# Optimization experiments

Hardware: AMD Instinct MI355X
Metric: run time of the kernel (lower is better)

Reference implementation:

```python
import jax, jax.numpy as jnp
import numpy as np

N_HEADS = 16


def setup_inputs() -> dict:
    key = jax.random.key(0)
    ks = jax.random.split(key, 6)
    B, S, E = 2, 2048, 1024
    scale = 1.0 / np.sqrt(E)
    return {
        "X": jax.random.normal(ks[0], (B, S, E), dtype=jnp.float32),
        "Wq": jax.random.normal(ks[1], (E, E), dtype=jnp.float32) * scale,
        "Wk": jax.random.normal(ks[2], (E, E), dtype=jnp.float32) * scale,
        "Wv": jax.random.normal(ks[3], (E, E), dtype=jnp.float32) * scale,
        "Wp": jax.random.normal(ks[4], (E, E), dtype=jnp.float32) * scale,
        "bp": jnp.zeros((E,), dtype=jnp.float32),
    }


def reference(X, Wq, Wk, Wv, Wp, bp):
    B, S, E = X.shape
    H = N_HEADS
    dk = E // H
    # qkv projections (Linear with weight [out,in] -> x @ W.T), split heads
    q = (X @ Wq.T).reshape(B, S, H, dk).transpose(0, 2, 1, 3)  # [B,H,S,dk]
    k = (X @ Wk.T).reshape(B, S, H, dk).transpose(0, 2, 1, 3)
    v = (X @ Wv.T).reshape(B, S, H, dk).transpose(0, 2, 1, 3)
    scores = jnp.einsum('bhqd,bhkd->bhqk', q, k) / jnp.sqrt(jnp.asarray(dk, X.dtype))
    causal = jnp.tril(jnp.ones((S, S), dtype=bool))  # [S,S]
    scores = jnp.where(causal[None, None], scores, jnp.asarray(-jnp.inf, X.dtype))
    attn = jax.nn.softmax(scores, axis=-1)  # [B,H,S,S]
    y = jnp.einsum('bhqk,bhkd->bhqd', attn, v)  # [B,H,S,dk]
    y = y.transpose(0, 2, 1, 3).reshape(B, S, E)
    return y @ Wp.T + bp
```

## Files before the change

kernel.cpp:

```cpp
#include <hip/hip_runtime.h>

typedef unsigned short u16;
typedef __bf16 bf16x8 __attribute__((ext_vector_type(8)));
typedef float f32x4 __attribute__((ext_vector_type(4)));
typedef unsigned short u16x8 __attribute__((ext_vector_type(8)));
typedef unsigned short u16x4 __attribute__((ext_vector_type(4)));

union B8 { u16x8 u; bf16x8 b; };

#define MFMA_BF16(a, b, c) __builtin_amdgcn_mfma_f32_16x16x32_bf16((a), (b), (c), 0, 0, 0)

__device__ __forceinline__ u16 f2bf(float f) {
  unsigned x = __float_as_uint(f);
  unsigned r = x + 0x7fffu + ((x >> 16) & 1u);
  return (u16)(r >> 16);
}

__device__ __forceinline__ unsigned cvt_pk_bf16(float lo, float hi) {
  unsigned r;
  asm("v_cvt_pk_bf16_f32 %0, %1, %2" : "=v"(r) : "v"(lo), "v"(hi));
  return r;
}

__device__ __forceinline__ void gl2lds16(const void* g, void* l) {
  __builtin_amdgcn_global_load_lds(
      (const __attribute__((address_space(1))) void*)g,
      (__attribute__((address_space(3))) void*)l, 16, 0, 0);
}

__global__ __launch_bounds__(256) void cast5_kernel(
    const float* __restrict__ X, const float* __restrict__ Wq,
    const float* __restrict__ Wk, const float* __restrict__ Wv,
    const float* __restrict__ Wp, u16* __restrict__ Xb, u16* __restrict__ Wqb,
    u16* __restrict__ Wkb, u16* __restrict__ Wvb, u16* __restrict__ Wpb) {
  size_t i = ((size_t)blockIdx.x * 256 + threadIdx.x) * 4;
  const float* src;
  u16* dst;
  size_t off;
  if (i < 4194304) {
    src = X; dst = Xb; off = i;
  } else if (i < 5242880) {
    src = Wq; dst = Wqb; off = i - 4194304;
  } else if (i < 6291456) {
    src = Wk; dst = Wkb; off = i - 5242880;
  } else if (i < 7340032) {
    src = Wv; dst = Wvb; off = i - 6291456;
  } else {
    src = Wp; dst = Wpb; off = i - 7340032;
  }
  float4 v = *(const float4*)(src + off);
  u16x4 o;
  o[0] = f2bf(v.x); o[1] = f2bf(v.y); o[2] = f2bf(v.z); o[3] = f2bf(v.w);
  *(u16x4*)(dst + off) = o;
}

template <int N0>
__device__ __forceinline__ void mfma16(f32x4 (&acc)[8][4], B8 (&af)[8], B8& b0,
                                       B8& b1) {
  __builtin_amdgcn_s_setprio(1);
#pragma unroll
  for (int m = 0; m < 8; ++m) {
    acc[m][N0] = MFMA_BF16(af[m].b, b0.b, acc[m][N0]);
    acc[m][N0 + 1] = MFMA_BF16(af[m].b, b1.b, acc[m][N0 + 1]);
  }
  __builtin_amdgcn_s_setprio(0);
}

__global__ __launch_bounds__(512, 2) void gemm_qkv256(
    const u16* __restrict__ Xb, const u16* __restrict__ Wb,
    u16* __restrict__ Qb, u16* __restrict__ Kb, u16* __restrict__ Vt) {
  __shared__ __align__(16) u16 Al[2][2][256 * 32];
  __shared__ __align__(16) u16 Bl[2][2][256 * 32];

  int tid = threadIdx.x, lane = tid & 63, w = tid >> 6;
  int wr = w >> 2, wc = w & 3;
  int l16 = lane & 15, lg = lane >> 4;

  int bid = blockIdx.x;
  int swz = (bid & 7) * 24 + (bid >> 3);
  int bm = swz / 12, bn = swz % 12;

  const u16* Ag = Xb + (size_t)bm * 256 * 1024;
  const u16* Bg = Wb + (size_t)bn * 256 * 1024;

  int srow = w * 16 + (lane >> 2);
  int scol = lane & 3;

  auto stA = [&](int buf, int kh, int kt) {
#pragma unroll
    for (int p2 = 0; p2 < 2; ++p2) {
      int r = p2 * 128 + srow;
      int sl = scol ^ ((r >> 1) & 3);
      gl2lds16(Ag + (size_t)r * 1024 + kt * 64 + kh * 32 + sl * 8,
               (char*)&Al[buf][kh][0] + (size_t)(p2 * 128 + w * 16) * 64);
    }
  };
  auto stB = [&](int buf, int kh, int kt) {
#pragma unroll
    for (int p2 = 0; p2 < 2; ++p2) {
      int r = p2 * 128 + srow;
      int sl = scol ^ ((r >> 1) & 3);
      gl2lds16(Bg + (size_t)r * 1024 + kt * 64 + kh * 32 + sl * 8,
               (char*)&Bl[buf][kh][0] + (size_t)(p2 * 128 + w * 16) * 64);
    }
  };
  auto ldA = [&](int buf, int kk, B8 (&af)[8]) {
#pragma unroll
    for (int m = 0; m < 8; ++m) {
      int r = wr * 128 + m * 16 + l16;
      af[m].u = *(const u16x8*)((const char*)&Al[buf][kk][0] + r * 64 +
                                ((lg ^ ((r >> 1) & 3)) << 4));
    }
  };
  auto ldB = [&](int buf, int kk, int nf, B8& bf) {
    int r = wc * 64 + nf * 16 + l16;
    bf.u = *(const u16x8*)((const char*)&Bl[buf][kk][0] + r * 64 +
                           ((lg ^ ((r >> 1) & 3)) << 4));
  };

  f32x4 acc[8][4] = {};

  stA(0, 0, 0); stB(0, 0, 0);
  stA(0, 1, 0); stB(0, 1, 0);
  stA(1, 0, 1); stB(1, 0, 1);
  asm volatile("s_waitcnt vmcnt(8)" ::: "memory");
  __builtin_amdgcn_s_barrier();

  B8 af[8], b0, b1;
  for (int I = 0; I < 8; ++I) {
    int p = 2 * I;
    bool last = (I == 7);
    stA(1, 1, p + 1);
    ldA(0, 0, af); ldB(0, 0, 0, b0); ldB(0, 0, 1, b1);
    mfma16<0>(acc, af, b0, b1);
    stB(1, 1, p + 1);
    ldB(0, 0, 2, b0); ldB(0, 0, 3, b1);
    mfma16<2>(acc, af, b0, b1);
    if (last) asm volatile("s_waitcnt vmcnt(0)" ::: "memory");
    else      asm volatile("s_waitcnt vmcnt(8)" ::: "memory");
    __builtin_amdgcn_s_barrier();
    if (!last) stA(0, 0, p + 2);
    ldA(0, 1, af); ldB(0, 1, 0, b0); ldB(0, 1, 1, b1);
    mfma16<0>(acc, af, b0, b1);
    if (!last) stB(0, 0, p + 2);
    ldB(0, 1, 2, b0); ldB(0, 1, 3, b1);
    mfma16<2>(acc, af, b0, b1);
    if (last) asm volatile("s_waitcnt vmcnt(0)" ::: "memory");
    else      asm volatile("s_waitcnt vmcnt(8)" ::: "memory");
    __builtin_amdgcn_s_barrier();
    if (!last) stA(0, 1, p + 2);
    ldA(1, 0, af); ldB(1, 0, 0, b0); ldB(1, 0, 1, b1);
    mfma16<0>(acc, af, b0, b1);
    if (!last) stB(0, 1, p + 2);
    ldB(1, 0, 2, b0); ldB(1, 0, 3, b1);
    mfma16<2>(acc, af, b0, b1);
    if (last) asm volatile("s_waitcnt vmcnt(0)" ::: "memory");
    else      asm volatile("s_waitcnt vmcnt(8)" ::: "memory");
    __builtin_amdgcn_s_barrier();
    if (!last) stA(1, 0, p + 3);
    ldA(1, 1, af); ldB(1, 1, 0, b0); ldB(1, 1, 1, b1);
    mfma16<0>(acc, af, b0, b1);
    if (!last) stB(1, 0, p + 3);
    ldB(1, 1, 2, b0); ldB(1, 1, 3, b1);
    mfma16<2>(acc, af, b0, b1);
    if (!last) {
      asm volatile("s_waitcnt vmcnt(8)" ::: "memory");
      __builtin_amdgcn_s_barrier();
    }
  }

  const float QSCALE = 0.18033688011112042f;
#pragma unroll
  for (int m = 0; m < 8; ++m)
#pragma unroll
    for (int nf = 0; nf < 4; ++nf) {
      int colg = bn * 256 + wc * 64 + nf * 16 + l16;
      int rowg = bm * 256 + wr * 128 + m * 16 + lg * 4;
      if (bn < 4) {
#pragma unroll
        for (int j = 0; j < 4; ++j)
          Qb[(size_t)(rowg + j) * 1024 + colg] = f2bf(acc[m][nf][j] * QSCALE);
      } else if (bn < 8) {
#pragma unroll
        for (int j = 0; j < 4; ++j)
          Kb[(size_t)(rowg + j) * 1024 + (colg - 1024)] = f2bf(acc[m][nf][j]);
      } else {
        int cv = colg - 2048;
        int hh = cv >> 6, d = cv & 63;
        int bb = rowg >> 11, s0 = rowg & 2047;
        u16x4 pk;
#pragma unroll
        for (int j = 0; j < 4; ++j) pk[j] = f2bf(acc[m][nf][j]);
        *(u16x4*)(Vt + ((size_t)(bb * 16 + hh) * 64 + d) * 2048 + s0) = pk;
      }
    }
}

__global__ __launch_bounds__(256) void gemm_proj_kernel(
    const u16* __restrict__ Y1, const u16* __restrict__ Wpb,
    float* __restrict__ out, const float* __restrict__ bias) {
  __shared__ __align__(16) u16 Asm[2][128 * 64];
  __shared__ __align__(16) u16 Bsm[2][128 * 64];

  const int Kd = 1024, N = 1024;
  int bid = blockIdx.x;
  int swz = (bid & 7) * 32 + (bid >> 3);
  int bm = swz >> 3, bn = swz & 7;
  int tid = threadIdx.x;
  int lane = tid & 63, w = tid >> 6;
  int wr = w >> 1, wc = w & 1;
  int l16 = lane & 15, lg = lane >> 4;

  const u16* Abase = Y1 + (size_t)bm * 128 * Kd;
  const u16* Bbase = Wpb + (size_t)bn * 128 * Kd;

  int r0 = tid >> 3;

  auto stage = [&](int buf, int kt) {
#pragma unroll
    for (int i = 0; i < 4; ++i) {
      int r = i * 32 + r0;
      int sl = (tid & 7) ^ (r & 7);
      gl2lds16(Abase + (size_t)r * Kd + kt * 64 + sl * 8,
               &Asm[buf][i * 2048 + w * 512]);
      gl2lds16(Bbase + (size_t)r * Kd + kt * 64 + sl * 8,
               &Bsm[buf][i * 2048 + w * 512]);
    }
  };

  f32x4 acc[4][4] = {};
  stage(0, 0);
  int buf = 0;

  for (int kt = 0; kt < 16; ++kt) {
    asm volatile("s_waitcnt vmcnt(0)" ::: "memory");
    __syncthreads();
    if (kt + 1 < 16) stage(buf ^ 1, kt + 1);

    B8 af[4][2], bfr[4][2];
#pragma unroll
    for (int mi = 0; mi < 4; ++mi)
#pragma unroll
      for (int kk = 0; kk < 2; ++kk) {
        int r = wr * 64 + mi * 16 + l16;
        int s = kk * 4 + lg;
        af[mi][kk].u = *(const u16x8*)((const char*)&Asm[buf][0] + r * 128 +
                                       ((s ^ (r & 7)) << 4));
      }
#pragma unroll
    for (int ni = 0; ni < 4; ++ni)
#pragma unroll
      for (int kk = 0; kk < 2; ++kk) {
        int r = wc * 64 + ni * 16 + l16;
        int s = kk * 4 + lg;
        bfr[ni][kk].u = *(const u16x8*)((const char*)&Bsm[buf][0] + r * 128 +
                                        ((s ^ (r & 7)) << 4));
      }
    __builtin_amdgcn_s_setprio(1);
#pragma unroll
    for (int mi = 0; mi < 4; ++mi)
#pragma unroll
      for (int ni = 0; ni < 4; ++ni) {
        acc[mi][ni] = MFMA_BF16(af[mi][0].b, bfr[ni][0].b, acc[mi][ni]);
        acc[mi][ni] = MFMA_BF16(af[mi][1].b, bfr[ni][1].b, acc[mi][ni]);
      }
    __builtin_amdgcn_s_setprio(0);
    buf ^= 1;
  }

#pragma unroll
  for (int mi = 0; mi < 4; ++mi)
#pragma unroll
    for (int ni = 0; ni < 4; ++ni) {
      int col = bn * 128 + wc * 64 + ni * 16 + l16;
#pragma unroll
      for (int j = 0; j < 4; ++j) {
        int row = bm * 128 + wr * 64 + mi * 16 + lg * 4 + j;
        out[(size_t)row * N + col] = acc[mi][ni][j] + bias[col];
      }
    }
}

__global__ __launch_bounds__(256, 4) void attn_kernel(const u16* __restrict__ Q,
                                                      const u16* __restrict__ K,
                                                      const u16* __restrict__ Vt,
                                                      u16* __restrict__ Y) {
  __shared__ __align__(16) u16 Kl[2][64 * 64];
  __shared__ __align__(16) u16 Vl[2][64 * 64];
  __shared__ __align__(16) u16 Pl[4][16 * 64];

  const int E = 1024, S = 2048;
  int tid = threadIdx.x;
  int lane = tid & 63, w = tid >> 6;
  int l16 = lane & 15, lg = lane >> 4;
  int h7 = l16 & 7;

  int bid = blockIdx.x;
  int bh = (bid & 7) * 4 + ((bid >> 3) & 3);
  int u = bid >> 5;
  int g = u & 7, kq = u >> 3;
  int qt = (kq == 0) ? 31 - g : (kq == 1) ? 16 + g : (kq == 2) ? 15 - g : g;
  int b = bh >> 4, h = bh & 15;

  const u16* Qb = Q + (size_t)b * S * E + (size_t)h * 64;
  const u16* Kb = K + (size_t)b * S * E + (size_t)h * 64;
  const u16* Vb = Vt + (size_t)bh * 64 * 2048;

  int r0 = tid >> 3;
  int s0 = (tid & 7) ^ (r0 & 7);
  size_t koff = (size_t)r0 * 1024 + s0 * 8;
  size_t voff = (size_t)r0 * 2048 + s0 * 8;
  const u16* kpA = Kb;
  const u16* kpB = Kb + 32 * 1024;
  const u16* vpA = Vb;
  const u16* vpB = Vb + 32 * 2048;

  const char* kbase0 = (const char*)&Kl[0][0] + l16 * 128 + ((lg ^ h7) << 4);
  const char* kbase1 = (const char*)&Kl[0][0] + l16 * 128 + (((4 + lg) ^ h7) << 4);
  const char* vbase0 = (const char*)&Vl[0][0] + l16 * 128 + ((lg ^ h7) << 4);
  const char* vbase1 = (const char*)&Vl[0][0] + l16 * 128 + (((4 + lg) ^ h7) << 4);
  char* pw0 = (char*)&Pl[w][0] + l16 * 128 + (((0 * 2 + (lg >> 1)) ^ h7) << 4) + (lg & 1) * 8;
  char* pw1 = (char*)&Pl[w][0] + l16 * 128 + (((1 * 2 + (lg >> 1)) ^ h7) << 4) + (lg & 1) * 8;
  char* pw2 = (char*)&Pl[w][0] + l16 * 128 + (((2 * 2 + (lg >> 1)) ^ h7) << 4) + (lg & 1) * 8;
  char* pw3 = (char*)&Pl[w][0] + l16 * 128 + (((3 * 2 + (lg >> 1)) ^ h7) << 4) + (lg & 1) * 8;
  const char* pr0 = (const char*)&Pl[w][0] + l16 * 128 + ((lg ^ h7) << 4);
  const char* pr1 = (const char*)&Pl[w][0] + l16 * 128 + (((4 + lg) ^ h7) << 4);

  B8 qa[2];
#pragma unroll
  for (int kk = 0; kk < 2; ++kk)
    qa[kk].u = *(const u16x8*)(Qb + (size_t)(qt * 64 + w * 16 + l16) * E + kk * 32 + lg * 8);

  f32x4 o[4] = {};
  float lrun = 0.f;
  int qrow = w * 16 + l16;

  gl2lds16(kpA + koff, &Kl[0][w * 512]);
  gl2lds16(vpA + voff, &Vl[0][w * 512]);
  gl2lds16(kpB + koff, &Kl[0][2048 + w * 512]);
  gl2lds16(vpB + voff, &Vl[0][2048 + w * 512]);
  kpA += 65536; kpB += 65536; vpA += 64; vpB += 64;

#define ATTN_ITER(BF, DOMASK, DOSTAGE)                                         \
  do {                                                                         \
    asm volatile("s_waitcnt vmcnt(0)" ::: "memory");                           \
    __syncthreads();                                                           \
    if (DOSTAGE) {                                                             \
      gl2lds16(kpA + koff, &Kl[(BF) ^ 1][w * 512]);                            \
      gl2lds16(vpA + voff, &Vl[(BF) ^ 1][w * 512]);                            \
      gl2lds16(kpB + koff, &Kl[(BF) ^ 1][2048 + w * 512]);                     \
      gl2lds16(vpB + voff, &Vl[(BF) ^ 1][2048 + w * 512]);                     \
      kpA += 65536; kpB += 65536; vpA += 64; vpB += 64;                        \
    }                                                                          \
    f32x4 sa[4] = {};                                                          \
    __builtin_amdgcn_s_setprio(1);                                             \
    _Pragma("unroll") for (int nb = 0; nb < 4; ++nb) {                         \
      B8 kf0, kf1;                                                             \
      kf0.u = *(const u16x8*)(kbase0 + (BF)*8192 + nb * 2048);                 \
      kf1.u = *(const u16x8*)(kbase1 + (BF)*8192 + nb * 2048);                 \
      sa[nb] = MFMA_BF16(kf0.b, qa[0].b, sa[nb]);                              \
      sa[nb] = MFMA_BF16(kf1.b, qa[1].b, sa[nb]);                              \
    }                                                                          \
    __builtin_amdgcn_s_setprio(0);                                             \
    float p[16];                                                               \
    _Pragma("unroll") for (int nb = 0; nb < 4; ++nb)                           \
        _Pragma("unroll") for (int j = 0; j < 4; ++j) {                        \
      float pe = __builtin_amdgcn_exp2f(sa[nb][j]);                            \
      if (DOMASK) {                                                            \
        int kv = nb * 16 + lg * 4 + j;                                         \
        if (kv > qrow) pe = 0.f;                                               \
      }                                                                        \
      p[nb * 4 + j] = pe;                                                      \
    }                                                                          \
    {                                                                          \
      union { u16x4 v; unsigned uu[2]; } pk;                                   \
      pk.uu[0] = cvt_pk_bf16(p[0], p[1]);                                      \
      pk.uu[1] = cvt_pk_bf16(p[2], p[3]);                                      \
      *(u16x4*)pw0 = pk.v;                                                     \
      pk.uu[0] = cvt_pk_bf16(p[4], p[5]);                                      \
      pk.uu[1] = cvt_pk_bf16(p[6], p[7]);                                      \
      *(u16x4*)pw1 = pk.v;                                                     \
      pk.uu[0] = cvt_pk_bf16(p[8], p[9]);                                      \
      pk.uu[1] = cvt_pk_bf16(p[10], p[11]);                                    \
      *(u16x4*)pw2 = pk.v;                                                     \
      pk.uu[0] = cvt_pk_bf16(p[12], p[13]);                                    \
      pk.uu[1] = cvt_pk_bf16(p[14], p[15]);                                    \
      *(u16x4*)pw3 = pk.v;                                                     \
    }                                                                          \
    lrun += ((p[0] + p[1]) + (p[2] + p[3])) + ((p[4] + p[5]) + (p[6] + p[7])) +\
            ((p[8] + p[9]) + (p[10] + p[11])) +                                \
            ((p[12] + p[13]) + (p[14] + p[15]));                               \
    B8 pa0, pa1;                                                               \
    pa0.u = *(const u16x8*)pr0;                                                \
    pa1.u = *(const u16x8*)pr1;                                                \
    asm volatile("s_waitcnt lgkmcnt(0)" ::: "memory");                         \
    __builtin_amdgcn_sched_barrier(0);                                         \
    __builtin_amdgcn_s_setprio(1);                                             \
    _Pragma("unroll") for (int nb = 0; nb < 4; ++nb) {                         \
      B8 vf0, vf1;                                                             \
      vf0.u = *(const u16x8*)(vbase0 + (BF)*8192 + nb * 2048);                 \
      vf1.u = *(const u16x8*)(vbase1 + (BF)*8192 + nb * 2048);                 \
      o[nb] = MFMA_BF16(pa0.b, vf0.b, o[nb]);                                  \
      o[nb] = MFMA_BF16(pa1.b, vf1.b, o[nb]);                                  \
    }                                                                          \
    __builtin_amdgcn_s_setprio(0);                                             \
  } while (0)

  int U = qt;
  int i = 0;
  for (; i + 2 <= U; i += 2) {
    ATTN_ITER(0, false, true);
    ATTN_ITER(1, false, true);
  }
  if (U & 1) {
    ATTN_ITER(0, false, true);
    ATTN_ITER(1, true, false);
  } else {
    ATTN_ITER(0, true, false);
  }
#undef ATTN_ITER

  lrun += __shfl_xor(lrun, 16);
  lrun += __shfl_xor(lrun, 32);
  float inv[4];
#pragma unroll
  for (int j = 0; j < 4; ++j) {
    float lj = __shfl(lrun, (lane & 48) | (lg * 4 + j));
    inv[j] = 1.0f / lj;
  }
#pragma unroll
  for (int nb = 0; nb < 4; ++nb)
#pragma unroll
    for (int j = 0; j < 4; ++j) {
      int row = qt * 64 + w * 16 + lg * 4 + j;
      int col = h * 64 + nb * 16 + l16;
      Y[((size_t)b * S + row) * E + col] = f2bf(o[nb][j] * inv[j]);
    }
}

extern "C" void kernel_launch(void* const* d_in, const int* in_sizes, int n_in,
                              void* d_out, int out_size, void* d_ws,
                              size_t ws_size, hipStream_t stream) {
  const float* X = (const float*)d_in[0];
  const float* Wq = (const float*)d_in[1];
  const float* Wk = (const float*)d_in[2];
  const float* Wv = (const float*)d_in[3];
  const float* Wp = (const float*)d_in[4];
  const float* bp = (const float*)d_in[5];
  float* out = (float*)d_out;

  char* ws = (char*)d_ws;
  const size_t MB = 1ull << 20;
  u16* Xb = (u16*)(ws + 0 * MB);
  u16* Wqb = (u16*)(ws + 8 * MB);
  u16* Wkb = (u16*)(ws + 10 * MB);
  u16* Wvb = (u16*)(ws + 12 * MB);
  u16* Wpb = (u16*)(ws + 14 * MB);
  u16* Qb = (u16*)(ws + 16 * MB);
  u16* Kb = (u16*)(ws + 24 * MB);
  u16* VtB = (u16*)(ws + 32 * MB);
  u16* Y1 = (u16*)(ws + 40 * MB);

  cast5_kernel<<<8192, 256, 0, stream>>>(X, Wq, Wk, Wv, Wp, Xb, Wqb, Wkb, Wvb, Wpb);
  gemm_qkv256<<<192, 512, 0, stream>>>(Xb, Wqb, Qb, Kb, VtB);
  attn_kernel<<<1024, 256, 0, stream>>>(Qb, Kb, VtB, Y1);
  gemm_proj_kernel<<<256, 256, 0, stream>>>(Y1, Wpb, out, bp);
}
```

Before: 105.4 us.

## Feed P directly from registers into PV MFMA using 16x16x16 bf16

Removes the per-wave LDS round trip for the probability tile P (write, wait, read back). The bf16-packed exponentials are used directly as A operands of 16x16x16 bf16 MFMAs, with V fragments read in a matching 4-element layout. This drops LDS traffic and the lgkmcnt wait, but doubles the number of PV MFMA instructions (16 smaller ones instead of 8) and uses narrower 8-byte LDS reads for V.

```diff
diff --git a/kernel.cpp b/kernel.cpp
--- a/kernel.cpp
+++ b/kernel.cpp
@@ -9,6 +9,10 @@
 union B8 { u16x8 u; bf16x8 b; };
 
 #define MFMA_BF16(a, b, c) __builtin_amdgcn_mfma_f32_16x16x32_bf16((a), (b), (c), 0, 0, 0)
+
+__device__ __forceinline__ void mfma16x16x16(f32x4& c, u16x4 a, u16x4 b) {
+  asm("v_mfma_f32_16x16x16_bf16 %0, %1, %2, %0" : "+v"(c) : "v"(a), "v"(b));
+}
 
 __device__ __forceinline__ u16 f2bf(float f) {
   unsigned x = __float_as_uint(f);
@@ -287,7 +291,6 @@
                                                       u16* __restrict__ Y) {
   __shared__ __align__(16) u16 Kl[2][64 * 64];
   __shared__ __align__(16) u16 Vl[2][64 * 64];
-  __shared__ __align__(16) u16 Pl[4][16 * 64];
 
   const int E = 1024, S = 2048;
   int tid = threadIdx.x;
@@ -317,14 +320,11 @@
 
   const char* kbase0 = (const char*)&Kl[0][0] + l16 * 128 + ((lg ^ h7) << 4);
   const char* kbase1 = (const char*)&Kl[0][0] + l16 * 128 + (((4 + lg) ^ h7) << 4);
-  const char* vbase0 = (const char*)&Vl[0][0] + l16 * 128 + ((lg ^ h7) << 4);
-  const char* vbase1 = (const char*)&Vl[0][0] + l16 * 128 + (((4 + lg) ^ h7) << 4);
-  char* pw0 = (char*)&Pl[w][0] + l16 * 128 + (((0 * 2 + (lg >> 1)) ^ h7) << 4) + (lg & 1) * 8;
-  char* pw1 = (char*)&Pl[w][0] + l16 * 128 + (((1 * 2 + (lg >> 1)) ^ h7) << 4) + (lg & 1) * 8;
-  char* pw2 = (char*)&Pl[w][0] + l16 * 128 + (((2 * 2 + (lg >> 1)) ^ h7) << 4) + (lg & 1) * 8;
-  char* pw3 = (char*)&Pl[w][0] + l16 * 128 + (((3 * 2 + (lg >> 1)) ^ h7) << 4) + (lg & 1) * 8;
-  const char* pr0 = (const char*)&Pl[w][0] + l16 * 128 + ((lg ^ h7) << 4);
-  const char* pr1 = (const char*)&Pl[w][0] + l16 * 128 + (((4 + lg) ^ h7) << 4);
+  const char* vb64[4];
+#pragma unroll
+  for (int kvs = 0; kvs < 4; ++kvs)
+    vb64[kvs] = (const char*)&Vl[0][0] + l16 * 128 +
+                (((kvs * 2 + (lg >> 1)) ^ h7) << 4) + (lg & 1) * 8;
 
   B8 qa[2];
 #pragma unroll
@@ -362,46 +362,33 @@
       sa[nb] = MFMA_BF16(kf1.b, qa[1].b, sa[nb]);                              \
     }                                                                          \
     __builtin_amdgcn_s_setprio(0);                                             \
-    float p[16];                                                               \
-    _Pragma("unroll") for (int nb = 0; nb < 4; ++nb)                           \
-        _Pragma("unroll") for (int j = 0; j < 4; ++j) {                        \
-      float pe = __builtin_amdgcn_exp2f(sa[nb][j]);                            \
+    u16x4 pa[4];                                                               \
+    float rs = 0.f;                                                            \
+    _Pragma("unroll") for (int nb = 0; nb < 4; ++nb) {                         \
+      float pe0 = __builtin_amdgcn_exp2f(sa[nb][0]);                           \
+      float pe1 = __builtin_amdgcn_exp2f(sa[nb][1]);                           \
+      float pe2 = __builtin_amdgcn_exp2f(sa[nb][2]);                           \
+      float pe3 = __builtin_amdgcn_exp2f(sa[nb][3]);                           \
       if (DOMASK) {                                                            \
-        int kv = nb * 16 + lg * 4 + j;                                         \
-        if (kv > qrow) pe = 0.f;                                               \
+        int kv0 = nb * 16 + lg * 4;                                            \
+        if (kv0 + 0 > qrow) pe0 = 0.f;                                         \
+        if (kv0 + 1 > qrow) pe1 = 0.f;                                         \
+        if (kv0 + 2 > qrow) pe2 = 0.f;                                         \
+        if (kv0 + 3 > qrow) pe3 = 0.f;                                         \
       }                                                                        \
-      p[nb * 4 + j] = pe;                                                      \
+      union { u16x4 v; unsigned uu[2]; } pk;                                   \
+      pk.uu[0] = cvt_pk_bf16(pe0, pe1);                                        \
+      pk.uu[1] = cvt_pk_bf16(pe2, pe3);                                        \
+      pa[nb] = pk.v;                                                           \
+      rs += (pe0 + pe1) + (pe2 + pe3);                                         \
     }                                                                          \
-    {                                                                          \
-      union { u16x4 v; unsigned uu[2]; } pk;                                   \
-      pk.uu[0] = cvt_pk_bf16(p[0], p[1]);                                      \
-      pk.uu[1] = cvt_pk_bf16(p[2], p[3]);                                      \
-      *(u16x4*)pw0 = pk.v;                                                     \
-      pk.uu[0] = cvt_pk_bf16(p[4], p[5]);                                      \
-      pk.uu[1] = cvt_pk_bf16(p[6], p[7]);                                      \
-      *(u16x4*)pw1 = pk.v;                                                     \
-      pk.uu[0] = cvt_pk_bf16(p[8], p[9]);                                      \
-      pk.uu[1] = cvt_pk_bf16(p[10], p[11]);                                    \
-      *(u16x4*)pw2 = pk.v;                                                     \
-      pk.uu[0] = cvt_pk_bf16(p[12], p[13]);                                    \
-      pk.uu[1] = cvt_pk_bf16(p[14], p[15]);                                    \
-      *(u16x4*)pw3 = pk.v;                                                     \
-    }                                                                          \
-    lrun += ((p[0] + p[1]) + (p[2] + p[3])) + ((p[4] + p[5]) + (p[6] + p[7])) +\
-            ((p[8] + p[9]) + (p[10] + p[11])) +                                \
-            ((p[12] + p[13]) + (p[14] + p[15]));                               \
-    B8 pa0, pa1;                                                               \
-    pa0.u = *(const u16x8*)pr0;                                                \
-    pa1.u = *(const u16x8*)pr1;                                                \
-    asm volatile("s_waitcnt lgkmcnt(0)" ::: "memory");                         \
-    __builtin_amdgcn_sched_barrier(0);                                         \
+    lrun += rs;                                                                \
     __builtin_amdgcn_s_setprio(1);                                             \
-    _Pragma("unroll") for (int nb = 0; nb < 4; ++nb) {                         \
-      B8 vf0, vf1;                                                             \
-      vf0.u = *(const u16x8*)(vbase0 + (BF)*8192 + nb * 2048);                 \
-      vf1.u = *(const u16x8*)(vbase1 + (BF)*8192 + nb * 2048);                 \
-      o[nb] = MFMA_BF16(pa0.b, vf0.b, o[nb]);                                  \
-      o[nb] = MFMA_BF16(pa1.b, vf1.b, o[nb]);                                  \
+    _Pragma("unroll") for (int kvs = 0; kvs < 4; ++kvs) {                      \
+      _Pragma("unroll") for (int nbd = 0; nbd < 4; ++nbd) {                    \
+        u16x4 vf = *(const u16x4*)(vb64[kvs] + (BF)*8192 + nbd * 2048);        \
+        mfma16x16x16(o[nbd], pa[kvs], vf);                                     \
+      }                                                                        \
     }                                                                          \
     __builtin_amdgcn_s_setprio(0);                                             \
   } while (0)
```

After: 106.3 us. About the same (+0.9%).
